# Optimization experiments

Hardware: AMD Instinct MI355X
Metric: run time of the kernel (lower is better)

The kernel has to match this reference:

```python
import jax, jax.numpy as jnp
import numpy as np

N_NODES = 50000
N_EDGES = 800000
N_REL = 3
N_GRAPHS = 500
EMB = 128
IN_DIM = EMB * 3
HID = 256
N_CLASS = 10
N_SHAPE, N_COLOR, MAX_POS = 8, 8, 128


def rgcn_layer(h, src, dst, etype, W, root, b):
    """PyG RGCNConv with default aggr='mean':
    out[v] = sum_r mean_{(j->v) in E_r} h[j] @ W[r] + h[v] @ root + b
    Aggregate raw features per (dst, relation) bucket, then apply relation matmuls.
    """
    N, R = h.shape[0], W.shape[0]
    seg = dst * R + etype  # combined (node, relation) segment id
    sums = jax.ops.segment_sum(h[src], seg, num_segments=N * R)          # (N*R, d)
    cnt = jax.ops.segment_sum(jnp.ones(seg.shape, h.dtype), seg, num_segments=N * R)
    mean = (sums / jnp.maximum(cnt, 1.0)[:, None]).reshape(N, R, -1)     # (N, R, d)
    return jnp.einsum('nrd,rdh->nh', mean, W) + h @ root + b


def setup_inputs() -> dict:
    key = jax.random.key(0)
    ks = jax.random.split(key, 20)
    f32 = jnp.float32
    inp = {
        's': jax.random.randint(ks[0], (N_NODES,), 0, N_SHAPE),
        'c': jax.random.randint(ks[1], (N_NODES,), 0, N_COLOR),
        'p': jax.random.randint(ks[2], (N_NODES,), 0, MAX_POS),
        'edge_index': jax.random.randint(ks[3], (2, N_EDGES), 0, N_NODES),
        'edge_type': jax.random.randint(ks[4], (N_EDGES,), 0, N_REL),
        'batch': jnp.sort(jax.random.randint(ks[5], (N_NODES,), 0, N_GRAPHS)),
        'shape_emb': jax.random.normal(ks[6], (N_SHAPE, EMB), f32),
        'color_emb': jax.random.normal(ks[7], (N_COLOR, EMB), f32),
        'pos_emb': jax.random.normal(ks[8], (MAX_POS, EMB), f32),
        'W1': jax.random.normal(ks[9], (N_REL, IN_DIM, HID), f32) / np.sqrt(IN_DIM),
        'root1': jax.random.normal(ks[10], (IN_DIM, HID), f32) / np.sqrt(IN_DIM),
        'b1': jnp.zeros((HID,), f32),
        'W2': jax.random.normal(ks[11], (N_REL, HID, HID), f32) / np.sqrt(HID),
        'root2': jax.random.normal(ks[12], (HID, HID), f32) / np.sqrt(HID),
        'b2': jnp.zeros((HID,), f32),
        'lin_w': jax.random.normal(ks[13], (HID, N_CLASS), f32) / np.sqrt(HID),
        'lin_b': jnp.zeros((N_CLASS,), f32),
    }
    return inp


def reference(s, c, p, edge_index, edge_type, batch,
              shape_emb, color_emb, pos_emb,
              W1, root1, b1, W2, root2, b2, lin_w, lin_b):
    src, dst = edge_index[0], edge_index[1]
    h = jnp.concatenate([shape_emb[s], color_emb[c], pos_emb[p]], axis=-1)  # (N, 3*emb)
    h = jax.nn.relu(rgcn_layer(h, src, dst, edge_type, W1, root1, b1))
    h = jax.nn.relu(rgcn_layer(h, src, dst, edge_type, W2, root2, b2))
    # global_mean_pool over graphs
    gsum = jax.ops.segment_sum(h, batch, num_segments=N_GRAPHS)
    gcnt = jax.ops.segment_sum(jnp.ones((h.shape[0],), h.dtype), batch, num_segments=N_GRAPHS)
    pooled = gsum / jnp.maximum(gcnt, 1.0)[:, None]
    return pooled @ lin_w + lin_b
```

## Files before the change

kernel.cpp:

```cpp
#include <hip/hip_runtime.h>
#include <hip/hip_bf16.h>

#define NN 50000
#define NE 800000
#define NR 3
#define NG 500
#define NB (NN * NR)
#define NCLS 10
#define NCMB 8192
#define CHUNK 2048
#define NBLK ((NB + CHUNK - 1) / CHUNK)

#define P1_COMBO   196
#define P1_ZCNT    586
#define P1_ZPOOL   502
#define P1_TAB     576
#define P1_WF      1024
#define P1_TOTAL   (P1_COMBO + P1_ZCNT + P1_ZPOOL + P1_TAB + P1_WF)
#define P2_CNT     3125
#define P2_COMB    (4 * NCMB)
#define P2_TOTAL   (P2_CNT + P2_COMB)

typedef __hip_bfloat16 bf16;
typedef __attribute__((ext_vector_type(8))) short short8;
typedef __attribute__((ext_vector_type(4))) float floatx4;

static __device__ __forceinline__ float b2f(bf16 x) { return __bfloat162float(x); }
static __device__ __forceinline__ bf16  f2b(float x) { return __float2bfloat16(x); }
static __device__ __forceinline__ float bs2f(short x) {
    return __bfloat162float(*reinterpret_cast<const bf16*>(&x));
}
static __device__ __forceinline__ short f2bs(float x) {
    bf16 b = __float2bfloat16(x);
    return *reinterpret_cast<const short*>(&b);
}

__global__ __launch_bounds__(256) void prep1(const int* __restrict__ s,
                                             const int* __restrict__ c,
                                             const int* __restrict__ p,
                                             const float* __restrict__ se,
                                             const float* __restrict__ ce,
                                             const float* __restrict__ pe,
                                             const float* __restrict__ W1,
                                             const float* __restrict__ root1,
                                             const float* __restrict__ W2,
                                             const float* __restrict__ root2,
                                             int* __restrict__ combo,
                                             unsigned* __restrict__ cnt,
                                             unsigned* __restrict__ poolz,
                                             float* __restrict__ tab,
                                             bf16* __restrict__ Wf) {
    int b = blockIdx.x, t = threadIdx.x;
    if (b < P1_COMBO) {
        int n = b * 256 + t;
        if (n < NN) combo[n] = (s[n] << 10) | (c[n] << 7) | p[n];
        return;
    }
    b -= P1_COMBO;
    if (b < P1_ZCNT) {
        int i = b * 256 + t;
        if (i < NB) cnt[i] = 0u;
        return;
    }
    b -= P1_ZCNT;
    if (b < P1_ZPOOL) {
        int i = b * 256 + t;
        if (i < NG * 256 + NG) poolz[i] = 0u;
        return;
    }
    b -= P1_ZPOOL;
    if (b < P1_TAB) {
        int r = b / 144, row = b % 144;
        const float* A; int segk;
        if (row < 8)       { A = se + row * 128;        segk = 0; }
        else if (row < 16) { A = ce + (row - 8) * 128;  segk = 128; }
        else               { A = pe + (row - 16) * 128; segk = 256; }
        const float* W = (r < 3) ? (W1 + (size_t)r * 384 * 256) : root1;
        float acc = 0.f;
        for (int k = 0; k < 128; ++k)
            acc += A[k] * W[(size_t)(segk + k) * 256 + t];
        tab[((size_t)r * 144 + row) * 256 + t] = acc;
        return;
    }
    b -= P1_TAB;
    {
        int idx = b * 256 + t;
        int j     = idx & 7;
        int lane  = (idx >> 3) & 63;
        int ni    = (idx >> 9) & 3;
        int chunk = (idx >> 11) & 31;
        int colblk = idx >> 16;
        int col = colblk * 64 + ni * 16 + (lane & 15);
        int k   = chunk * 32 + (lane >> 4) * 8 + j;
        float v = (k < 768) ? W2[((size_t)(k >> 8) * 256 + (k & 255)) * 256 + col]
                            : root2[(size_t)(k - 768) * 256 + col];
        Wf[idx] = f2b(v);
    }
}

__global__ __launch_bounds__(256) void prep2(const int* __restrict__ ei,
                                             const int* __restrict__ et,
                                             int* __restrict__ cnt,
                                             const float* __restrict__ tab,
                                             const float* __restrict__ b1,
                                             bf16* __restrict__ comb) {
    int b = blockIdx.x, t = threadIdx.x;
    if (b < P2_CNT) {
        int e = b * 256 + t;
        if (e < NE) atomicAdd(&cnt[ei[NE + e] * NR + et[e]], 1);
        return;
    }
    b -= P2_CNT;
    {
        int r = b >> 13, cmb = b & (NCMB - 1);
        int si = cmb >> 10, ci = (cmb >> 7) & 7, pi = cmb & 127;
        const float* tr = tab + (size_t)r * 144 * 256;
        float v = tr[si * 256 + t] + tr[(8 + ci) * 256 + t] + tr[(16 + pi) * 256 + t];
        if (r == 3) v += b1[t];
        comb[(size_t)b * 256 + t] = f2b(v);
    }
}

__global__ __launch_bounds__(256) void scan_block_sums(const int* __restrict__ cnt,
                                                       int* __restrict__ bsum) {
    __shared__ int sm[256];
    int b = blockIdx.x, t = threadIdx.x;
    int base = b * CHUNK + t * 8, s = 0;
#pragma unroll
    for (int j = 0; j < 8; ++j) { int i = base + j; if (i < NB) s += cnt[i]; }
    sm[t] = s; __syncthreads();
    for (int st = 128; st; st >>= 1) { if (t < st) sm[t] += sm[t + st]; __syncthreads(); }
    if (!t) bsum[b] = sm[0];
}

__global__ __launch_bounds__(256) void scan_write(const int* __restrict__ cnt,
                                                  const int* __restrict__ bsum,
                                                  int* __restrict__ off,
                                                  int* __restrict__ cursor) {
    int b = blockIdx.x, t = threadIdx.x;
    int bbase = 0;
    for (int i = 0; i < b; ++i) bbase += bsum[i];
    if (b == 0 && t == 0) {
        int tot = 0;
        for (int i = 0; i < NBLK; ++i) tot += bsum[i];
        off[NB] = tot;
    }
    int base = b * CHUNK + t * 8;
    int v[8], ts = 0;
#pragma unroll
    for (int j = 0; j < 8; ++j) { int i = base + j; v[j] = (i < NB) ? cnt[i] : 0; ts += v[j]; }
    int lane = t & 63, wv = t >> 6;
    int incl = ts;
    for (int d = 1; d < 64; d <<= 1) {
        int o = __shfl_up(incl, d, 64);
        if (lane >= d) incl += o;
    }
    __shared__ int wsum[4];
    if (lane == 63) wsum[wv] = incl;
    __syncthreads();
    int wbase = 0;
    for (int w = 0; w < wv; ++w) wbase += wsum[w];
    int run = bbase + wbase + incl - ts;
#pragma unroll
    for (int j = 0; j < 8; ++j) {
        int i = base + j;
        if (i < NB) { off[i] = run; cursor[i] = run; }
        run += v[j];
    }
}

__global__ __launch_bounds__(256) void scatter_edges(const int* __restrict__ ei,
                                                     const int* __restrict__ et,
                                                     const int* __restrict__ combo,
                                                     int* __restrict__ cursor,
                                                     int* __restrict__ eidx,
                                                     int* __restrict__ ecmb) {
    int e = blockIdx.x * 256 + threadIdx.x;
    if (e >= NE) return;
    int b = ei[NE + e] * NR + et[e];
    int pos = atomicAdd(&cursor[b], 1);
    int s = ei[e];
    eidx[pos] = s;
    ecmb[pos] = combo[s];
}

__global__ __launch_bounds__(256) void l1_fused(const int* __restrict__ off,
                                                const int* __restrict__ ecmb,
                                                const int* __restrict__ combo,
                                                const bf16* __restrict__ comb,
                                                bf16* __restrict__ h1) {
    int wave = threadIdx.x >> 6, lane = threadIdx.x & 63;
    int dst = blockIdx.x * 4 + wave;
    if (dst >= NN) return;
    int half = lane >> 5, li8 = (lane & 31) * 8;
    float acc[8];
    if (half == 0) {
        int cmbD = combo[dst];
        short8 rv = *(const short8*)(comb + ((size_t)(3 * NCMB) + cmbD) * 256 + li8);
#pragma unroll
        for (int i = 0; i < 8; ++i) acc[i] = bs2f(rv[i]);
    } else {
#pragma unroll
        for (int i = 0; i < 8; ++i) acc[i] = 0.f;
    }
    for (int r = 0; r < NR; ++r) {
        int lo = off[dst * NR + r], hi = off[dst * NR + r + 1];
        if (hi <= lo) continue;
        const bf16* cr = comb + (size_t)r * NCMB * 256;
        float s[8] = {};
        int j = lo;
        for (; j + 8 <= hi; j += 8) {
            int c0 = ecmb[j + half],     c1 = ecmb[j + 2 + half];
            int c2 = ecmb[j + 4 + half], c3 = ecmb[j + 6 + half];
            short8 v0 = *(const short8*)(cr + (size_t)c0 * 256 + li8);
            short8 v1 = *(const short8*)(cr + (size_t)c1 * 256 + li8);
            short8 v2 = *(const short8*)(cr + (size_t)c2 * 256 + li8);
            short8 v3 = *(const short8*)(cr + (size_t)c3 * 256 + li8);
#pragma unroll
            for (int i = 0; i < 8; ++i)
                s[i] += (bs2f(v0[i]) + bs2f(v1[i])) + (bs2f(v2[i]) + bs2f(v3[i]));
        }
        for (; j + 2 <= hi; j += 2) {
            int c0 = ecmb[j + half];
            short8 v0 = *(const short8*)(cr + (size_t)c0 * 256 + li8);
#pragma unroll
            for (int i = 0; i < 8; ++i) s[i] += bs2f(v0[i]);
        }
        if (j < hi && half == 0) {
            short8 v0 = *(const short8*)(cr + (size_t)ecmb[j] * 256 + li8);
#pragma unroll
            for (int i = 0; i < 8; ++i) s[i] += bs2f(v0[i]);
        }
        float inv = 1.0f / (float)(hi - lo);
#pragma unroll
        for (int i = 0; i < 8; ++i) {
            float tot = s[i] + __shfl_xor(s[i], 32);
            if (half == 0) acc[i] += tot * inv;
        }
    }
    if (half == 0) {
        short8 o;
#pragma unroll
        for (int i = 0; i < 8; ++i) o[i] = f2bs(fmaxf(acc[i], 0.f));
        *(short8*)(h1 + (size_t)dst * 256 + li8) = o;
    }
}

__global__ __launch_bounds__(256) void agg_all(const int* __restrict__ off,
                                               const int* __restrict__ eidx,
                                               const bf16* __restrict__ h1,
                                               bf16* __restrict__ hagg) {
    int wave = threadIdx.x >> 6, lane = threadIdx.x & 63;
    int dst = blockIdx.x * 4 + wave;
    if (dst >= NN) return;
    int half = lane >> 5, li8 = (lane & 31) * 8;
    for (int r = 0; r < NR; ++r) {
        int lo = off[dst * NR + r], hi = off[dst * NR + r + 1];
        float s[8] = {};
        int j = lo;
        for (; j + 8 <= hi; j += 8) {
            int e0 = eidx[j + half],     e1 = eidx[j + 2 + half];
            int e2 = eidx[j + 4 + half], e3 = eidx[j + 6 + half];
            short8 v0 = *(const short8*)(h1 + (size_t)e0 * 256 + li8);
            short8 v1 = *(const short8*)(h1 + (size_t)e1 * 256 + li8);
            short8 v2 = *(const short8*)(h1 + (size_t)e2 * 256 + li8);
            short8 v3 = *(const short8*)(h1 + (size_t)e3 * 256 + li8);
#pragma unroll
            for (int i = 0; i < 8; ++i)
                s[i] += (bs2f(v0[i]) + bs2f(v1[i])) + (bs2f(v2[i]) + bs2f(v3[i]));
        }
        for (; j + 2 <= hi; j += 2) {
            int e0 = eidx[j + half];
            short8 v0 = *(const short8*)(h1 + (size_t)e0 * 256 + li8);
#pragma unroll
            for (int i = 0; i < 8; ++i) s[i] += bs2f(v0[i]);
        }
        if (j < hi && half == 0) {
            short8 v0 = *(const short8*)(h1 + (size_t)eidx[j] * 256 + li8);
#pragma unroll
            for (int i = 0; i < 8; ++i) s[i] += bs2f(v0[i]);
        }
        float inv = (hi > lo) ? 1.0f / (float)(hi - lo) : 0.f;
        short8 o;
#pragma unroll
        for (int i = 0; i < 8; ++i) {
            float tot = s[i] + __shfl_xor(s[i], 32);
            o[i] = f2bs(tot * inv);
        }
        if (half == 0)
            *(short8*)(hagg + (size_t)dst * 768 + r * 256 + li8) = o;
    }
}

__global__ __launch_bounds__(256) void gemm_cat(const bf16* __restrict__ hagg,
                                                const bf16* __restrict__ h1,
                                                const bf16* __restrict__ Wf,
                                                const float* __restrict__ bias,
                                                bf16* __restrict__ h2) {
    __shared__ short lds[4][2][32 * 40];
    const int t = threadIdx.x;
    const int wave = t >> 6, lane = t & 63;
    const int quad = lane >> 4, l16 = lane & 15;
    const int row0 = blockIdx.x * 32;
    const int colblk = wave;
    const int rsub = lane >> 2;
    const int ksub = (lane & 3) * 8;
    short* A0 = lds[wave][0];
    short* A1 = lds[wave][1];

    const int r0 = min(row0 + rsub, NN - 1);
    const int r1 = min(row0 + 16 + rsub, NN - 1);
    const bf16* gA0 = hagg + (size_t)r0 * 768 + ksub;
    const bf16* gA1 = hagg + (size_t)r1 * 768 + ksub;
    const bf16* gH0 = h1 + (size_t)r0 * 256 + ksub;
    const bf16* gH1 = h1 + (size_t)r1 * 256 + ksub;
    const short8* bbase = (const short8*)Wf + (size_t)colblk * 32 * 4 * 64 + lane;

    auto loadA2 = [&](int k0, short8& a0, short8& a1) {
        if (k0 < 768) { a0 = *(const short8*)(gA0 + k0); a1 = *(const short8*)(gA1 + k0); }
        else          { a0 = *(const short8*)(gH0 + k0 - 768); a1 = *(const short8*)(gH1 + k0 - 768); }
    };
    auto loadB = [&](int chunk, short8* bf4) {
        const short8* bp = bbase + (size_t)chunk * 4 * 64;
#pragma unroll
        for (int ni = 0; ni < 4; ++ni) bf4[ni] = bp[ni * 64];
    };

    floatx4 acc[2][4] = {};
    short8 aE0, aE1, bE[4];
    short8 aO0, aO1, bO[4];
    loadA2(0, aE0, aE1);  loadB(0, bE);
    loadA2(32, aO0, aO1); loadB(1, bO);

#pragma unroll
    for (int i = 0; i < 32; i += 2) {
        *(short8*)&A0[rsub * 40 + ksub] = aE0;
        *(short8*)&A0[(16 + rsub) * 40 + ksub] = aE1;
        {
            short8 af0 = *(const short8*)&A0[l16 * 40 + quad * 8];
            short8 af1 = *(const short8*)&A0[(16 + l16) * 40 + quad * 8];
#pragma unroll
            for (int ni = 0; ni < 4; ++ni) {
                acc[0][ni] = __builtin_amdgcn_mfma_f32_16x16x32_bf16(af0, bE[ni], acc[0][ni], 0, 0, 0);
                acc[1][ni] = __builtin_amdgcn_mfma_f32_16x16x32_bf16(af1, bE[ni], acc[1][ni], 0, 0, 0);
            }
        }
        if (i + 2 < 32) { loadA2((i + 2) * 32, aE0, aE1); loadB(i + 2, bE); }
        *(short8*)&A1[rsub * 40 + ksub] = aO0;
        *(short8*)&A1[(16 + rsub) * 40 + ksub] = aO1;
        {
            short8 af0 = *(const short8*)&A1[l16 * 40 + quad * 8];
            short8 af1 = *(const short8*)&A1[(16 + l16) * 40 + quad * 8];
#pragma unroll
            for (int ni = 0; ni < 4; ++ni) {
                acc[0][ni] = __builtin_amdgcn_mfma_f32_16x16x32_bf16(af0, bO[ni], acc[0][ni], 0, 0, 0);
                acc[1][ni] = __builtin_amdgcn_mfma_f32_16x16x32_bf16(af1, bO[ni], acc[1][ni], 0, 0, 0);
            }
        }
        if (i + 3 < 32) { loadA2((i + 3) * 32, aO0, aO1); loadB(i + 3, bO); }
    }

#pragma unroll
    for (int mi = 0; mi < 2; ++mi) {
#pragma unroll
        for (int ni = 0; ni < 4; ++ni) {
            int n = colblk * 64 + ni * 16 + l16;
            float bn = bias[n];
#pragma unroll
            for (int ii = 0; ii < 4; ++ii) {
                int gm = row0 + mi * 16 + quad * 4 + ii;
                if (gm < NN) {
                    float v = acc[mi][ni][ii] + bn;
                    h2[(size_t)gm * 256 + n] = f2b(fmaxf(v, 0.f));
                }
            }
        }
    }
}

#define PN 64
__global__ __launch_bounds__(256) void pool_rle(const int* __restrict__ batch,
                                                const bf16* __restrict__ H,
                                                float* __restrict__ pool,
                                                float* __restrict__ gcnt) {
    int t = threadIdx.x;
    int n0 = blockIdx.x * PN;
    int nend = n0 + PN; if (nend > NN) nend = NN;
    int curg = batch[n0];
    float acc = 0.f, cnt = 0.f;
    for (int n = n0; n < nend; ++n) {
        int g = batch[n];
        if (g != curg) {
            atomicAdd(&pool[(size_t)curg * 256 + t], acc);
            if (t == 0) atomicAdd(&gcnt[curg], cnt);
            acc = 0.f; cnt = 0.f; curg = g;
        }
        acc += b2f(H[(size_t)n * 256 + t]);
        cnt += 1.f;
    }
    atomicAdd(&pool[(size_t)curg * 256 + t], acc);
    if (t == 0) atomicAdd(&gcnt[curg], cnt);
}

__global__ __launch_bounds__(256) void final_head(const float* __restrict__ pool,
                                                  const float* __restrict__ gcnt,
                                                  const float* __restrict__ lin_w,
                                                  const float* __restrict__ lin_b,
                                                  float* __restrict__ out) {
    __shared__ float sm[256];
    int g = blockIdx.x, t = threadIdx.x;
    float inv = 1.0f / fmaxf(gcnt[g], 1.0f);
    sm[t] = pool[(size_t)g * 256 + t] * inv;
    __syncthreads();
    if (t < NCLS) {
        float s = lin_b[t];
        for (int d = 0; d < 256; ++d) s += sm[d] * lin_w[d * NCLS + t];
        out[g * NCLS + t] = s;
    }
}

extern "C" void kernel_launch(void* const* d_in, const int* in_sizes, int n_in,
                              void* d_out, int out_size, void* d_ws, size_t ws_size,
                              hipStream_t stream) {
    const int*   s_idx = (const int*)d_in[0];
    const int*   c_idx = (const int*)d_in[1];
    const int*   p_idx = (const int*)d_in[2];
    const int*   ei    = (const int*)d_in[3];
    const int*   et    = (const int*)d_in[4];
    const int*   batch = (const int*)d_in[5];
    const float* se    = (const float*)d_in[6];
    const float* ce    = (const float*)d_in[7];
    const float* pe    = (const float*)d_in[8];
    const float* W1    = (const float*)d_in[9];
    const float* root1 = (const float*)d_in[10];
    const float* b1    = (const float*)d_in[11];
    const float* W2    = (const float*)d_in[12];
    const float* root2 = (const float*)d_in[13];
    const float* b2    = (const float*)d_in[14];
    const float* lin_w = (const float*)d_in[15];
    const float* lin_b = (const float*)d_in[16];
    float* out = (float*)d_out;

    char* w = (char*)d_ws;
    size_t o = 0;
    auto alloc = [&](size_t bytes) -> void* {
        o = (o + 15) & ~(size_t)15;
        void* ptr = w + o;
        o += bytes;
        return ptr;
    };
    bf16*  hagg   = (bf16*) alloc((size_t)NN * 768 * 2);
    bf16*  h1     = (bf16*) alloc((size_t)NN * 256 * 2);
    bf16*  h2     = (bf16*) alloc((size_t)NN * 256 * 2);
    bf16*  comb   = (bf16*) alloc((size_t)4 * NCMB * 256 * 2);
    int*   combo  = (int*)  alloc((size_t)NN * 4);
    int*   eidx   = (int*)  alloc((size_t)NE * 4);
    int*   ecmb   = (int*)  alloc((size_t)NE * 4);
    int*   cnt    = (int*)  alloc((size_t)NB * 4);
    int*   off    = (int*)  alloc((size_t)(NB + 1) * 4);
    int*   cursor = (int*)  alloc((size_t)NB * 4);
    int*   bsum   = (int*)  alloc((size_t)NBLK * 4);
    float* tab    = (float*)alloc((size_t)4 * 144 * 256 * 4);
    bf16*  Wf     = (bf16*) alloc((size_t)256 * 1024 * 2);
    float* pool   = (float*)alloc((size_t)NG * 256 * 4);
    float* gcnt   = (float*)alloc((size_t)NG * 4);
    (void)ws_size;

    prep1<<<P1_TOTAL, 256, 0, stream>>>(s_idx, c_idx, p_idx, se, ce, pe,
                                        W1, root1, W2, root2,
                                        combo, (unsigned*)cnt, (unsigned*)pool, tab, Wf);
    prep2<<<P2_TOTAL, 256, 0, stream>>>(ei, et, cnt, tab, b1, comb);
    scan_block_sums<<<NBLK, 256, 0, stream>>>(cnt, bsum);
    scan_write<<<NBLK, 256, 0, stream>>>(cnt, bsum, off, cursor);
    scatter_edges<<<(NE + 255) / 256, 256, 0, stream>>>(ei, et, combo, cursor, eidx, ecmb);
    l1_fused<<<(NN + 3) / 4, 256, 0, stream>>>(off, ecmb, combo, comb, h1);
    agg_all<<<(NN + 3) / 4, 256, 0, stream>>>(off, eidx, h1, hagg);
    gemm_cat<<<(NN + 31) / 32, 256, 0, stream>>>(hagg, h1, Wf, b2, h2);
    pool_rle<<<(NN + PN - 1) / PN, 256, 0, stream>>>(batch, h2, pool, gcnt);
    final_head<<<NG, 256, 0, stream>>>(pool, gcnt, lin_w, lin_b, out);
}
```

Measured before the change: 411.9 us.

## Fuse layer-2 neighbor aggregation into the GEMM via an LDS-staged A tile

Merges agg_all and gemm_cat into one kernel. Each block gathers and averages neighbor features for its 32 rows across all 3 relations, along with each row's own h1 row, into a 64KB XOR-swizzled LDS tile. The MFMA GEMM then reads A straight from LDS. This removes the 77MB hagg round-trip through global memory and one launch. In exchange, the 64KB of LDS per block limits occupancy, and the GEMM cannot start until the gather finishes, so the gather's load latency may be less hidden.

```diff
diff --git a/kernel.cpp b/kernel.cpp
--- a/kernel.cpp
+++ b/kernel.cpp
@@ -246,125 +246,103 @@
     }
 }
 
-__global__ __launch_bounds__(256) void agg_all(const int* __restrict__ off,
-                                               const int* __restrict__ eidx,
-                                               const bf16* __restrict__ h1,
-                                               bf16* __restrict__ hagg) {
-    int wave = threadIdx.x >> 6, lane = threadIdx.x & 63;
-    int dst = blockIdx.x * 4 + wave;
-    if (dst >= NN) return;
-    int half = lane >> 5, li8 = (lane & 31) * 8;
-    for (int r = 0; r < NR; ++r) {
-        int lo = off[dst * NR + r], hi = off[dst * NR + r + 1];
-        float s[8] = {};
-        int j = lo;
-        for (; j + 8 <= hi; j += 8) {
-            int e0 = eidx[j + half],     e1 = eidx[j + 2 + half];
-            int e2 = eidx[j + 4 + half], e3 = eidx[j + 6 + half];
-            short8 v0 = *(const short8*)(h1 + (size_t)e0 * 256 + li8);
-            short8 v1 = *(const short8*)(h1 + (size_t)e1 * 256 + li8);
-            short8 v2 = *(const short8*)(h1 + (size_t)e2 * 256 + li8);
-            short8 v3 = *(const short8*)(h1 + (size_t)e3 * 256 + li8);
-#pragma unroll
-            for (int i = 0; i < 8; ++i)
-                s[i] += (bs2f(v0[i]) + bs2f(v1[i])) + (bs2f(v2[i]) + bs2f(v3[i]));
-        }
-        for (; j + 2 <= hi; j += 2) {
-            int e0 = eidx[j + half];
-            short8 v0 = *(const short8*)(h1 + (size_t)e0 * 256 + li8);
-#pragma unroll
-            for (int i = 0; i < 8; ++i) s[i] += bs2f(v0[i]);
-        }
-        if (j < hi && half == 0) {
-            short8 v0 = *(const short8*)(h1 + (size_t)eidx[j] * 256 + li8);
-#pragma unroll
-            for (int i = 0; i < 8; ++i) s[i] += bs2f(v0[i]);
-        }
-        float inv = (hi > lo) ? 1.0f / (float)(hi - lo) : 0.f;
-        short8 o;
-#pragma unroll
-        for (int i = 0; i < 8; ++i) {
-            float tot = s[i] + __shfl_xor(s[i], 32);
-            o[i] = f2bs(tot * inv);
-        }
-        if (half == 0)
-            *(short8*)(hagg + (size_t)dst * 768 + r * 256 + li8) = o;
-    }
-}
-
-__global__ __launch_bounds__(256) void gemm_cat(const bf16* __restrict__ hagg,
+__global__ __launch_bounds__(256) void agg_gemm(const int* __restrict__ off,
+                                                const int* __restrict__ eidx,
                                                 const bf16* __restrict__ h1,
                                                 const bf16* __restrict__ Wf,
                                                 const float* __restrict__ bias,
                                                 bf16* __restrict__ h2) {
-    __shared__ short lds[4][2][32 * 40];
+    __shared__ short Alds[32 * 1024];
     const int t = threadIdx.x;
     const int wave = t >> 6, lane = t & 63;
+    const int half = lane >> 5, l32 = lane & 31;
+    const int row0 = blockIdx.x * 32;
+
+#pragma unroll
+    for (int it = 0; it < 4; ++it) {
+        int lrow = wave * 8 + it * 2 + half;
+        int dst = row0 + lrow;
+        short8 v = {};
+        if (dst < NN) v = *(const short8*)(h1 + (size_t)dst * 256 + l32 * 8);
+        *(short8*)&Alds[lrow * 1024 + (((96 + l32) ^ (lrow & 7)) * 8)] = v;
+    }
+    for (int i = 0; i < 12; ++i) {
+        int bidx = wave * 24 + i * 2 + half;
+        int lrow = bidx / 3, r = bidx % 3;
+        int dst = row0 + lrow;
+        float s[8] = {};
+        float inv = 0.f;
+        if (dst < NN) {
+            int bk = dst * NR + r;
+            int lo = off[bk], hi = off[bk + 1];
+            if (hi > lo) {
+                int j = lo;
+                for (; j + 4 <= hi; j += 4) {
+                    int e0 = eidx[j], e1 = eidx[j + 1], e2 = eidx[j + 2], e3 = eidx[j + 3];
+                    short8 v0 = *(const short8*)(h1 + (size_t)e0 * 256 + l32 * 8);
+                    short8 v1 = *(const short8*)(h1 + (size_t)e1 * 256 + l32 * 8);
+                    short8 v2 = *(const short8*)(h1 + (size_t)e2 * 256 + l32 * 8);
+                    short8 v3 = *(const short8*)(h1 + (size_t)e3 * 256 + l32 * 8);
+#pragma unroll
+                    for (int q = 0; q < 8; ++q)
+                        s[q] += (bs2f(v0[q]) + bs2f(v1[q])) + (bs2f(v2[q]) + bs2f(v3[q]));
+                }
+                for (; j < hi; ++j) {
+                    short8 v0 = *(const short8*)(h1 + (size_t)eidx[j] * 256 + l32 * 8);
+#pragma unroll
+                    for (int q = 0; q < 8; ++q) s[q] += bs2f(v0[q]);
+                }
+                inv = 1.0f / (float)(hi - lo);
+            }
+        }
+        short8 o;
+#pragma unroll
+        for (int q = 0; q < 8; ++q) o[q] = f2bs(s[q] * inv);
+        *(short8*)&Alds[lrow * 1024 + (((r * 32 + l32) ^ (lrow & 7)) * 8)] = o;
+    }
+    __syncthreads();
+
     const int quad = lane >> 4, l16 = lane & 15;
-    const int row0 = blockIdx.x * 32;
-    const int colblk = wave;
-    const int rsub = lane >> 2;
-    const int ksub = (lane & 3) * 8;
-    short* A0 = lds[wave][0];
-    short* A1 = lds[wave][1];
-
-    const int r0 = min(row0 + rsub, NN - 1);
-    const int r1 = min(row0 + 16 + rsub, NN - 1);
-    const bf16* gA0 = hagg + (size_t)r0 * 768 + ksub;
-    const bf16* gA1 = hagg + (size_t)r1 * 768 + ksub;
-    const bf16* gH0 = h1 + (size_t)r0 * 256 + ksub;
-    const bf16* gH1 = h1 + (size_t)r1 * 256 + ksub;
-    const short8* bbase = (const short8*)Wf + (size_t)colblk * 32 * 4 * 64 + lane;
-
-    auto loadA2 = [&](int k0, short8& a0, short8& a1) {
-        if (k0 < 768) { a0 = *(const short8*)(gA0 + k0); a1 = *(const short8*)(gA1 + k0); }
-        else          { a0 = *(const short8*)(gH0 + k0 - 768); a1 = *(const short8*)(gH1 + k0 - 768); }
-    };
-    auto loadB = [&](int chunk, short8* bf4) {
-        const short8* bp = bbase + (size_t)chunk * 4 * 64;
+    const short8* bbase = (const short8*)Wf + (size_t)wave * (32 * 4 * 64) + lane;
+    auto loadB = [&](int c, short8* bf4) {
+        const short8* bp = bbase + (size_t)c * 256;
 #pragma unroll
         for (int ni = 0; ni < 4; ++ni) bf4[ni] = bp[ni * 64];
     };
+    auto ldA = [&](int row, int c) -> short8 {
+        return *(const short8*)&Alds[row * 1024 + ((((c << 2) + quad) ^ (row & 7)) * 8)];
+    };
 
     floatx4 acc[2][4] = {};
-    short8 aE0, aE1, bE[4];
-    short8 aO0, aO1, bO[4];
-    loadA2(0, aE0, aE1);  loadB(0, bE);
-    loadA2(32, aO0, aO1); loadB(1, bO);
-
-#pragma unroll
-    for (int i = 0; i < 32; i += 2) {
-        *(short8*)&A0[rsub * 40 + ksub] = aE0;
-        *(short8*)&A0[(16 + rsub) * 40 + ksub] = aE1;
+    short8 bE[4], bO[4];
+    loadB(0, bE); loadB(1, bO);
+#pragma unroll
+    for (int c = 0; c < 32; c += 2) {
         {
-            short8 af0 = *(const short8*)&A0[l16 * 40 + quad * 8];
-            short8 af1 = *(const short8*)&A0[(16 + l16) * 40 + quad * 8];
+            short8 a0 = ldA(l16, c), a1 = ldA(16 + l16, c);
 #pragma unroll
             for (int ni = 0; ni < 4; ++ni) {
-                acc[0][ni] = __builtin_amdgcn_mfma_f32_16x16x32_bf16(af0, bE[ni], acc[0][ni], 0, 0, 0);
-                acc[1][ni] = __builtin_amdgcn_mfma_f32_16x16x32_bf16(af1, bE[ni], acc[1][ni], 0, 0, 0);
+                acc[0][ni] = __builtin_amdgcn_mfma_f32_16x16x32_bf16(a0, bE[ni], acc[0][ni], 0, 0, 0);
+                acc[1][ni] = __builtin_amdgcn_mfma_f32_16x16x32_bf16(a1, bE[ni], acc[1][ni], 0, 0, 0);
             }
         }
-        if (i + 2 < 32) { loadA2((i + 2) * 32, aE0, aE1); loadB(i + 2, bE); }
-        *(short8*)&A1[rsub * 40 + ksub] = aO0;
-        *(short8*)&A1[(16 + rsub) * 40 + ksub] = aO1;
+        if (c + 2 < 32) loadB(c + 2, bE);
         {
-            short8 af0 = *(const short8*)&A1[l16 * 40 + quad * 8];
-            short8 af1 = *(const short8*)&A1[(16 + l16) * 40 + quad * 8];
+            short8 a0 = ldA(l16, c + 1), a1 = ldA(16 + l16, c + 1);
 #pragma unroll
             for (int ni = 0; ni < 4; ++ni) {
-                acc[0][ni] = __builtin_amdgcn_mfma_f32_16x16x32_bf16(af0, bO[ni], acc[0][ni], 0, 0, 0);
-                acc[1][ni] = __builtin_amdgcn_mfma_f32_16x16x32_bf16(af1, bO[ni], acc[1][ni], 0, 0, 0);
+                acc[0][ni] = __builtin_amdgcn_mfma_f32_16x16x32_bf16(a0, bO[ni], acc[0][ni], 0, 0, 0);
+                acc[1][ni] = __builtin_amdgcn_mfma_f32_16x16x32_bf16(a1, bO[ni], acc[1][ni], 0, 0, 0);
             }
         }
-        if (i + 3 < 32) { loadA2((i + 3) * 32, aO0, aO1); loadB(i + 3, bO); }
+        if (c + 3 < 32) loadB(c + 3, bO);
     }
 
 #pragma unroll
     for (int mi = 0; mi < 2; ++mi) {
 #pragma unroll
         for (int ni = 0; ni < 4; ++ni) {
-            int n = colblk * 64 + ni * 16 + l16;
+            int n = wave * 64 + ni * 16 + l16;
             float bn = bias[n];
 #pragma unroll
             for (int ii = 0; ii < 4; ++ii) {
@@ -449,7 +427,6 @@
         o += bytes;
         return ptr;
     };
-    bf16*  hagg   = (bf16*) alloc((size_t)NN * 768 * 2);
     bf16*  h1     = (bf16*) alloc((size_t)NN * 256 * 2);
     bf16*  h2     = (bf16*) alloc((size_t)NN * 256 * 2);
     bf16*  comb   = (bf16*) alloc((size_t)4 * NCMB * 256 * 2);
@@ -474,8 +451,7 @@
     scan_write<<<NBLK, 256, 0, stream>>>(cnt, bsum, off, cursor);
     scatter_edges<<<(NE + 255) / 256, 256, 0, stream>>>(ei, et, combo, cursor, eidx, ecmb);
     l1_fused<<<(NN + 3) / 4, 256, 0, stream>>>(off, ecmb, combo, comb, h1);
-    agg_all<<<(NN + 3) / 4, 256, 0, stream>>>(off, eidx, h1, hagg);
-    gemm_cat<<<(NN + 31) / 32, 256, 0, stream>>>(hagg, h1, Wf, b2, h2);
+    agg_gemm<<<(NN + 31) / 32, 256, 0, stream>>>(off, eidx, h1, Wf, b2, h2);
     pool_rle<<<(NN + PN - 1) / PN, 256, 0, stream>>>(batch, h2, pool, gcnt);
     final_head<<<NG, 256, 0, stream>>>(pool, gcnt, lin_w, lin_b, out);
 }
```

After: 491.5 us. 1.19x slower.

## Fuse mean-pool into GEMM epilogue and merge scan passes into one kernel

Applied to the files above, without the earlier changes.

The second-layer GEMM now stages its ReLU output tile in LDS and performs the run-length graph pooling with atomics directly, so the h2 buffer is never written and the separate pool kernel is gone. The two-kernel scan is merged into one kernel where each block recomputes its prefix base by reducing all preceding counts. This removes two launches and the h2 round trip through memory. In exchange, the scan does quadratic redundant reads of the count array (later blocks read up to 150K ints each) and the GEMM epilogue gains extra barriers plus an LDS transpose.

```diff
diff --git a/kernel.cpp b/kernel.cpp
--- a/kernel.cpp
+++ b/kernel.cpp
@@ -121,30 +121,20 @@
     }
 }
 
-__global__ __launch_bounds__(256) void scan_block_sums(const int* __restrict__ cnt,
-                                                       int* __restrict__ bsum) {
-    __shared__ int sm[256];
-    int b = blockIdx.x, t = threadIdx.x;
-    int base = b * CHUNK + t * 8, s = 0;
-#pragma unroll
-    for (int j = 0; j < 8; ++j) { int i = base + j; if (i < NB) s += cnt[i]; }
-    sm[t] = s; __syncthreads();
-    for (int st = 128; st; st >>= 1) { if (t < st) sm[t] += sm[t + st]; __syncthreads(); }
-    if (!t) bsum[b] = sm[0];
-}
-
 __global__ __launch_bounds__(256) void scan_write(const int* __restrict__ cnt,
-                                                  const int* __restrict__ bsum,
                                                   int* __restrict__ off,
                                                   int* __restrict__ cursor) {
+    __shared__ int sred[256];
+    __shared__ int wsum[4];
     int b = blockIdx.x, t = threadIdx.x;
-    int bbase = 0;
-    for (int i = 0; i < b; ++i) bbase += bsum[i];
-    if (b == 0 && t == 0) {
-        int tot = 0;
-        for (int i = 0; i < NBLK; ++i) tot += bsum[i];
-        off[NB] = tot;
-    }
+    long lim = (long)b * CHUNK;
+    int partial = 0;
+    for (long i = t; i < lim; i += 256) partial += cnt[i];
+    sred[t] = partial;
+    __syncthreads();
+    for (int st = 128; st; st >>= 1) { if (t < st) sred[t] += sred[t + st]; __syncthreads(); }
+    int bbase = sred[0];
+
     int base = b * CHUNK + t * 8;
     int v[8], ts = 0;
 #pragma unroll
@@ -155,11 +145,12 @@
         int o = __shfl_up(incl, d, 64);
         if (lane >= d) incl += o;
     }
-    __shared__ int wsum[4];
     if (lane == 63) wsum[wv] = incl;
     __syncthreads();
     int wbase = 0;
     for (int w = 0; w < wv; ++w) wbase += wsum[w];
+    if (b == NBLK - 1 && t == 0)
+        off[NB] = bbase + wsum[0] + wsum[1] + wsum[2] + wsum[3];
     int run = bbase + wbase + incl - ts;
 #pragma unroll
     for (int j = 0; j < 8; ++j) {
@@ -296,7 +287,9 @@
                                                 const bf16* __restrict__ h1,
                                                 const bf16* __restrict__ Wf,
                                                 const float* __restrict__ bias,
-                                                bf16* __restrict__ h2) {
+                                                const int* __restrict__ batch,
+                                                float* __restrict__ pool,
+                                                float* __restrict__ gcnt) {
     __shared__ short lds[4][2][32 * 40];
     const int t = threadIdx.x;
     const int wave = t >> 6, lane = t & 63;
@@ -360,6 +353,8 @@
         if (i + 3 < 32) { loadA2((i + 3) * 32, aO0, aO1); loadB(i + 3, bO); }
     }
 
+    __syncthreads();
+    short* st = &lds[0][0][0];
 #pragma unroll
     for (int mi = 0; mi < 2; ++mi) {
 #pragma unroll
@@ -368,38 +363,28 @@
             float bn = bias[n];
 #pragma unroll
             for (int ii = 0; ii < 4; ++ii) {
-                int gm = row0 + mi * 16 + quad * 4 + ii;
-                if (gm < NN) {
-                    float v = acc[mi][ni][ii] + bn;
-                    h2[(size_t)gm * 256 + n] = f2b(fmaxf(v, 0.f));
-                }
+                int lrow = mi * 16 + quad * 4 + ii;
+                float v = (row0 + lrow < NN) ? fmaxf(acc[mi][ni][ii] + bn, 0.f) : 0.f;
+                st[lrow * 260 + n] = f2bs(v);
             }
         }
     }
-}
-
-#define PN 64
-__global__ __launch_bounds__(256) void pool_rle(const int* __restrict__ batch,
-                                                const bf16* __restrict__ H,
-                                                float* __restrict__ pool,
-                                                float* __restrict__ gcnt) {
-    int t = threadIdx.x;
-    int n0 = blockIdx.x * PN;
-    int nend = n0 + PN; if (nend > NN) nend = NN;
-    int curg = batch[n0];
-    float acc = 0.f, cnt = 0.f;
-    for (int n = n0; n < nend; ++n) {
-        int g = batch[n];
+    __syncthreads();
+    int nrows = NN - row0; if (nrows > 32) nrows = 32;
+    int curg = batch[row0];
+    float a = 0.f, cntf = 0.f;
+    for (int rr = 0; rr < nrows; ++rr) {
+        int g = batch[row0 + rr];
         if (g != curg) {
-            atomicAdd(&pool[(size_t)curg * 256 + t], acc);
-            if (t == 0) atomicAdd(&gcnt[curg], cnt);
-            acc = 0.f; cnt = 0.f; curg = g;
-        }
-        acc += b2f(H[(size_t)n * 256 + t]);
-        cnt += 1.f;
-    }
-    atomicAdd(&pool[(size_t)curg * 256 + t], acc);
-    if (t == 0) atomicAdd(&gcnt[curg], cnt);
+            atomicAdd(&pool[(size_t)curg * 256 + t], a);
+            if (t == 0) atomicAdd(&gcnt[curg], cntf);
+            a = 0.f; cntf = 0.f; curg = g;
+        }
+        a += bs2f(st[rr * 260 + t]);
+        cntf += 1.f;
+    }
+    atomicAdd(&pool[(size_t)curg * 256 + t], a);
+    if (t == 0) atomicAdd(&gcnt[curg], cntf);
 }
 
 __global__ __launch_bounds__(256) void final_head(const float* __restrict__ pool,
@@ -451,7 +436,6 @@
     };
     bf16*  hagg   = (bf16*) alloc((size_t)NN * 768 * 2);
     bf16*  h1     = (bf16*) alloc((size_t)NN * 256 * 2);
-    bf16*  h2     = (bf16*) alloc((size_t)NN * 256 * 2);
     bf16*  comb   = (bf16*) alloc((size_t)4 * NCMB * 256 * 2);
     int*   combo  = (int*)  alloc((size_t)NN * 4);
     int*   eidx   = (int*)  alloc((size_t)NE * 4);
@@ -459,7 +443,6 @@
     int*   cnt    = (int*)  alloc((size_t)NB * 4);
     int*   off    = (int*)  alloc((size_t)(NB + 1) * 4);
     int*   cursor = (int*)  alloc((size_t)NB * 4);
-    int*   bsum   = (int*)  alloc((size_t)NBLK * 4);
     float* tab    = (float*)alloc((size_t)4 * 144 * 256 * 4);
     bf16*  Wf     = (bf16*) alloc((size_t)256 * 1024 * 2);
     float* pool   = (float*)alloc((size_t)NG * 256 * 4);
@@ -470,12 +453,10 @@
                                         W1, root1, W2, root2,
                                         combo, (unsigned*)cnt, (unsigned*)pool, tab, Wf);
     prep2<<<P2_TOTAL, 256, 0, stream>>>(ei, et, cnt, tab, b1, comb);
-    scan_block_sums<<<NBLK, 256, 0, stream>>>(cnt, bsum);
-    scan_write<<<NBLK, 256, 0, stream>>>(cnt, bsum, off, cursor);
+    scan_write<<<NBLK, 256, 0, stream>>>(cnt, off, cursor);
     scatter_edges<<<(NE + 255) / 256, 256, 0, stream>>>(ei, et, combo, cursor, eidx, ecmb);
     l1_fused<<<(NN + 3) / 4, 256, 0, stream>>>(off, ecmb, combo, comb, h1);
     agg_all<<<(NN + 3) / 4, 256, 0, stream>>>(off, eidx, h1, hagg);
-    gemm_cat<<<(NN + 31) / 32, 256, 0, stream>>>(hagg, h1, Wf, b2, h2);
-    pool_rle<<<(NN + PN - 1) / PN, 256, 0, stream>>>(batch, h2, pool, gcnt);
+    gemm_cat<<<(NN + 31) / 32, 256, 0, stream>>>(hagg, h1, Wf, b2, batch, pool, gcnt);
     final_head<<<NG, 256, 0, stream>>>(pool, gcnt, lin_w, lin_b, out);
 }
```

Measured after the change: 458.2 us. +11.2%, slower.
